# Kernel optimization log

Hardware: AMD Instinct MI355X
Metric: run time of the kernel (lower is better)

The kernel has to match this reference:

```python
import jax, jax.numpy as jnp
import numpy as np


def conv1x1(x, w, b):
    # x: [B,C,H,W], w: [O,C], b: [O]
    return jnp.einsum('bchw,oc->bohw', x, w) + b[None, :, None, None]


def conv2d_same(x, w, b):
    # x: [B,C,H,W], w: [O,I,kh,kw]
    y = jax.lax.conv_general_dilated(x, w, (1, 1), 'SAME',
                                     dimension_numbers=('NCHW', 'OIHW', 'NCHW'))
    return y + b[None, :, None, None]


def l2norm_c(x):
    # F.normalize(x, dim=1): x / max(||x||_2, eps)
    n = jnp.sqrt(jnp.sum(x * x, axis=1, keepdims=True))
    return x / jnp.maximum(n, 1e-12)


def warp_volume(k, disps, directs):
    # Plane-sweep warp. grid_sample(bilinear, border, align_corners=True) with a
    # pure horizontal shift: y-coords equal the identity grid exactly, so
    # bilinear interpolation reduces to 1-D interpolation along W.
    # k: [B,C,H,W], disps: [D], directs: [B,1,1,1] -> [B,C,H,W,D]
    B, C, H, W = k.shape
    dt = k.dtype
    base = jnp.arange(W, dtype=dt)                                   # pixel x
    # normalized shift disp*2 maps to disp*(W-1) pixels (align_corners=True)
    shift = disps.astype(dt)[None, :, None] * directs.reshape(B, 1, 1) * (W - 1)
    px = jnp.clip(base[None, None, :] + shift, 0.0, W - 1)            # [B,D,W] (border pad)
    x0 = jnp.floor(px).astype(jnp.int32)
    x1 = jnp.minimum(x0 + 1, W - 1)
    f = (px - x0.astype(dt))[:, None, None, :, :]                     # [B,1,1,D,W]
    gather = jax.vmap(lambda xb, ib: xb[:, :, ib])                    # [B,C,H,D,W]
    g0 = gather(k, x0)
    g1 = gather(k, x1)
    wk = g0 * (1.0 - f) + g1 * f                                      # [B,C,H,D,W]
    return jnp.transpose(wk, (0, 1, 2, 4, 3))                         # [B,C,H,W,D]


def setup_inputs() -> dict:
    key = jax.random.key(0)
    ks = jax.random.split(key, 16)
    B, C, H, W = 4, 128, 96, 320
    Cm, D = C // 4, 32
    f32 = jnp.float32
    inp = {
        't_feat': jax.random.normal(ks[0], (B, C, H, W), f32),
        's_feat': jax.random.normal(ks[1], (B, C, H, W), f32),
        'directs': jnp.ones((B, 1, 1, 1), f32),
        'image_shape': 320,
        'disps': jnp.arange(D, dtype=f32) * 0.01,
        'wq': jax.random.normal(ks[2], (Cm, C), f32) * 0.05,
        'bq': jnp.zeros((Cm,), f32),
        'wkc': jax.random.normal(ks[3], (Cm, C), f32) * 0.05,
        'bkc': jnp.zeros((Cm,), f32),
        'metric': jnp.eye(Cm, dtype=f32),
        'alpha': jnp.asarray(10.0, f32),
        'beta': jnp.asarray(0.0, f32),
        'w_cf': jax.random.normal(ks[4], (1, 1, 3, 3), f32) * 0.1,
        'b_cf': jnp.zeros((1,), f32),
        'w_da': jax.random.normal(ks[5], (D, 2 * Cm), f32) * 0.05,
        'b_da': jnp.zeros((D,), f32),
        'w_ex': jax.random.normal(ks[6], (C, D), f32) * 0.05,
        'b_ex': jnp.zeros((C,), f32),
        'w_fg': jax.random.normal(ks[7], (1, 2 * C), f32) * 0.05,
        'b_fg': jnp.zeros((1,), f32),
        'w_rd': jax.random.normal(ks[8], (C, C, 3, 3), f32) * 0.02,
        'b_rd': jnp.zeros((C,), f32),
        'w_se1': jax.random.normal(ks[9], (C // 16, C), f32) * 0.1,
        'w_se2': jax.random.normal(ks[10], (C, C // 16), f32) * 0.1,
    }
    return inp


def reference(t_feat, s_feat, directs, image_shape, disps,
              wq, bq, wkc, bkc, metric, alpha, beta,
              w_cf, b_cf, w_da, b_da, w_ex, b_ex, w_fg, b_fg,
              w_rd, b_rd, w_se1, w_se2):
    del image_shape  # only used when train_image_size is set (it is None here)
    q = l2norm_c(conv1x1(t_feat, wq, bq))          # [B,Cm,H,W]
    k = l2norm_c(conv1x1(s_feat, wkc, bkc))        # [B,Cm,H,W]
    warped = warp_volume(k, disps, directs)        # [B,Cm,H,W,D]
    M = 0.5 * (metric + metric.T)
    q_proj = jnp.einsum('bchw,cd->bdhw', q, M)
    sim = jnp.einsum('bdhw,bdhwk->bhwk', q_proj, warped)
    sim = jnp.tanh(alpha * sim + beta)             # [B,H,W,D]
    Cv = jnp.transpose(sim, (0, 3, 1, 2))          # [B,D,H,W]
    B, D, H, W = Cv.shape
    # Conv3d(1,1,(1,3,3)) == per-slice 2D 3x3 conv
    Cf = conv2d_same(Cv.reshape(B * D, 1, H, W), w_cf, b_cf).reshape(B, D, H, W)
    k_mean = warped.mean(axis=-1)                  # [B,Cm,H,W]
    da = jax.nn.sigmoid(conv1x1(jnp.concatenate([q, k_mean], axis=1), w_da, b_da))
    Cf = Cf * da
    P = jax.nn.softmax(Cf, axis=1)                 # [B,D,H,W]
    cost_feat = conv1x1(P, w_ex, b_ex)             # [B,C,H,W]
    g = jax.nn.sigmoid(conv1x1(jnp.concatenate([t_feat, cost_feat], axis=1), w_fg, b_fg))
    fused = g * t_feat + (1.0 - g) * cost_feat
    x = conv2d_same(fused, w_rd, b_rd)
    # SELayer(reduction=16)
    y = x.mean(axis=(2, 3))                        # [B,C]
    y = jax.nn.relu(y @ w_se1.T)
    y = jax.nn.sigmoid(y @ w_se2.T)
    x = x * y[:, :, None, None]
    x = jax.nn.elu(x)
    return (x, P)
```

## Files before the change

### kernel.cpp

```cpp
#include <hip/hip_runtime.h>
#include <hip/hip_bf16.h>
#include <math.h>


typedef __hip_bfloat16 bf16;
typedef unsigned short u16;
typedef __attribute__((ext_vector_type(8))) __bf16 bf16x8;
typedef __attribute__((ext_vector_type(4))) float f4;

#define DEVI static __device__ __forceinline__
DEVI float bf2f(bf16 x) { return __bfloat162float(x); }
DEVI bf16  f2bf(float x) { return __float2bfloat16(x); }
DEVI u16 bfbits(float x) { bf16 h = f2bf(x); return *(u16*)&h; }
DEVI float sigmoidf_(float x) { return 1.0f / (1.0f + expf(-x)); }

constexpr int B_ = 4, C_ = 128, H_ = 96, W_ = 320, CM = 32, D_ = 32;
constexpr int HW = H_ * W_;
constexpr int QPLANE = CM * HW;
constexpr int XN = B_ * C_ * HW;
constexpr int PLN = B_ * D_ * HW;

__device__ __align__(16) float g_scratch[8 * PLN];
__device__ __align__(16) u16   g_fused[XN];
__device__ __align__(16) u16   g_wt[9 * 128 * 128];
__device__ float g_ysum[512];
__device__ float g_se[512];
__device__ int   g_flag[1];

DEVI float ldin(const void* p, int i, int isb) {
    float v;
    if (isb) v = bf2f(((const bf16*)p)[i]);
    else     v = ((const float*)p)[i];
    return v;
}
DEVI void stout(void* p, int i, float v, int isb) {
    if (isb) ((bf16*)p)[i] = f2bf(v);
    else     ((float*)p)[i] = v;
}

__global__ __launch_bounds__(256) void k_detect(
    const void* __restrict__ t, const void* __restrict__ wqp)
{
    __shared__ int bad;
    int tid = threadIdx.x;
    if (tid == 0) bad = 0;
    __syncthreads();
    int mybad = 0;
    for (int i = tid; i < 4096; i += 256) {
        float v = bf2f(((const bf16*)t)[i]);
        if (!(v == v) || fabsf(v) > 64.0f) mybad = 1;
        float u = bf2f(((const bf16*)wqp)[i]);
        if (!(u == u) || fabsf(u) > 64.0f) mybad = 1;
    }
    if (mybad) atomicOr(&bad, 1);
    g_ysum[tid] = 0.f;
    g_ysum[tid + 256] = 0.f;
    __syncthreads();
    if (tid == 0) g_flag[0] = bad ? 0 : 1;
}

__global__ __launch_bounds__(256) void k_wprep(
    const void* __restrict__ w_rd, u16* __restrict__ gw)
{
    int isb = g_flag[0];
    int i = blockIdx.x * 256 + threadIdx.x;
    if (i >= 9 * 128 * 128) return;
    int pos = i >> 14, rem = i & 16383, co = rem >> 7, ci = rem & 127;
    gw[i] = bfbits(ldin(w_rd, (co * 128 + ci) * 9 + pos, isb));
}

__global__ __launch_bounds__(320) void k_qk(
    const void* __restrict__ t_feat, const void* __restrict__ s_feat,
    const void* __restrict__ wq, const void* __restrict__ bq,
    const void* __restrict__ wkc, const void* __restrict__ bkc,
    float* __restrict__ qout, float* __restrict__ kout)
{
    __shared__ float WST[C_ * CM];
    __shared__ float BS[CM];
    int isb = g_flag[0];
    int h = blockIdx.x, b = blockIdx.y, which = blockIdx.z;
    const void* in = which ? s_feat : t_feat;
    const void* wm = which ? wkc : wq;
    const void* bb = which ? bkc : bq;
    float* out = which ? kout : qout;
    int tid = threadIdx.x;
    for (int i = tid; i < C_ * CM; i += 320) {
        int o = i >> 7, c = i & 127;
        WST[c * CM + o] = ldin(wm, i, isb);
    }
    if (tid < CM) BS[tid] = ldin(bb, tid, isb);
    __syncthreads();
    int w = tid;
    float acc[CM];
    #pragma unroll
    for (int o = 0; o < CM; o++) acc[o] = BS[o];
    int base = (b * C_) * HW + h * W_ + w;
    for (int c = 0; c < C_; c++) {
        float v = ldin(in, base + c * HW, isb);
        #pragma unroll
        for (int o = 0; o < CM; o++) acc[o] += v * WST[c * CM + o];
    }
    float n = 0.f;
    #pragma unroll
    for (int o = 0; o < CM; o++) n += acc[o] * acc[o];
    float s = 1.0f / fmaxf(sqrtf(n), 1e-12f);
    float* op = out + (b * CM) * HW + h * W_ + w;
    #pragma unroll
    for (int o = 0; o < CM; o++) op[o * HW] = acc[o] * s;
}

__global__ __launch_bounds__(320, 3) void k_cost(
    const float* __restrict__ qbuf, const float* __restrict__ kbuf,
    const void* __restrict__ metric, const void* __restrict__ disps,
    const void* __restrict__ directs, const void* __restrict__ alpha_p,
    const void* __restrict__ beta_p, const void* __restrict__ w_da,
    const void* __restrict__ b_da,
    float* __restrict__ Cv, float* __restrict__ da)
{
    __shared__ float KS[CM][W_];
    __shared__ float MS[CM][CM];
    __shared__ float WDA[D_ * 64];
    __shared__ float BDA[D_];
    __shared__ float SH[D_];
    int isb = g_flag[0];
    int h = blockIdx.x, b = blockIdx.y, tid = threadIdx.x, w = tid;
    for (int i = tid; i < CM * CM; i += 320) {
        int c = i >> 5, d = i & 31;
        MS[c][d] = 0.5f * (ldin(metric, c * CM + d, isb) + ldin(metric, d * CM + c, isb));
    }
    for (int i = tid; i < D_ * 64; i += 320) WDA[i] = ldin(w_da, i, isb);
    if (tid < D_) {
        BDA[tid] = ldin(b_da, tid, isb);
        SH[tid] = ldin(disps, tid, isb) * ldin(directs, b, isb) * (float)(W_ - 1);
    }
    const float* kp = kbuf + b * QPLANE + h * W_;
    for (int c = 0; c < CM; c++) KS[c][w] = kp[c * HW + w];
    __syncthreads();

    float qp[CM], dqa[CM];
    #pragma unroll
    for (int d = 0; d < CM; d++) { qp[d] = 0.f; dqa[d] = 0.f; }
    const float* qpp = qbuf + b * QPLANE + h * W_ + w;
    for (int c = 0; c < CM; c++) {
        float v = qpp[c * HW];
        #pragma unroll
        for (int d = 0; d < CM; d++) qp[d] += v * MS[c][d];
        #pragma unroll
        for (int d = 0; d < D_; d++) dqa[d] += v * WDA[d * 64 + c];
    }

    float km[CM];
    #pragma unroll
    for (int c = 0; c < CM; c++) km[c] = 0.f;
    float alpha = ldin(alpha_p, 0, isb), beta = ldin(beta_p, 0, isb);
    float* cvp = Cv + (b * D_) * HW + h * W_ + w;
    for (int d = 0; d < D_; d++) {
        float px = fminf(fmaxf((float)w + SH[d], 0.f), (float)(W_ - 1));
        int x0 = (int)floorf(px);
        int x1 = min(x0 + 1, W_ - 1);
        float f = px - (float)x0;
        float sim = 0.f;
        #pragma unroll
        for (int c = 0; c < CM; c++) {
            float g0 = KS[c][x0], g1 = KS[c][x1];
            float val = g0 * (1.0f - f) + g1 * f;
            sim += qp[c] * val;
            km[c] += val;
        }
        cvp[d * HW] = tanhf(alpha * sim + beta);
    }

    #pragma unroll
    for (int c = 0; c < CM; c++) km[c] *= (1.0f / (float)D_);
    float* dap = da + (b * D_) * HW + h * W_ + w;
    for (int d = 0; d < D_; d++) {
        float s = BDA[d] + dqa[d];
        #pragma unroll
        for (int c = 0; c < CM; c++) s += WDA[d * 64 + 32 + c] * km[c];
        dap[d * HW] = sigmoidf_(s);
    }
}

__global__ __launch_bounds__(320) void k_cf_softmax(
    const float* __restrict__ Cv, const float* __restrict__ da,
    const void* __restrict__ w_cf, const void* __restrict__ b_cf,
    float* __restrict__ Pf, void* __restrict__ dout)
{
    __shared__ float R[3][322];
    int isb = g_flag[0];
    int h = blockIdx.x, b = blockIdx.y, tid = threadIdx.x, w = tid;
    float wcf[9];
    #pragma unroll
    for (int i = 0; i < 9; i++) wcf[i] = ldin(w_cf, i, isb);
    float bcf = ldin(b_cf, 0, isb);
    float vals[D_];
    for (int d = 0; d < D_; d++) {
        const float* base = Cv + ((b * D_ + d) * H_) * W_;
        #pragma unroll
        for (int r = 0; r < 3; r++) {
            int hh = h + r - 1;
            R[r][w + 1] = (hh >= 0 && hh < H_) ? base[hh * W_ + w] : 0.f;
        }
        if (tid == 0) {
            R[0][0] = R[1][0] = R[2][0] = 0.f;
            R[0][321] = R[1][321] = R[2][321] = 0.f;
        }
        __syncthreads();
        float s = bcf;
        #pragma unroll
        for (int r = 0; r < 3; r++)
            #pragma unroll
            for (int kw = 0; kw < 3; kw++)
                s += R[r][w + kw] * wcf[r * 3 + kw];
        vals[d] = s * da[((b * D_ + d) * H_ + h) * W_ + w];
        __syncthreads();
    }
    float m = vals[0];
    #pragma unroll
    for (int d = 1; d < D_; d++) m = fmaxf(m, vals[d]);
    float sum = 0.f;
    #pragma unroll
    for (int d = 0; d < D_; d++) { vals[d] = expf(vals[d] - m); sum += vals[d]; }
    float inv = 1.0f / sum;
    int o = (b * D_) * HW + h * W_ + w;
    #pragma unroll
    for (int d = 0; d < D_; d++) {
        float p = vals[d] * inv;
        Pf[o + d * HW] = p;
        stout(dout, XN + o + d * HW, p, isb);
    }
}

__global__ __launch_bounds__(320) void k_fuse(
    const float* __restrict__ Pf, const void* __restrict__ t_feat,
    const void* __restrict__ w_ex, const void* __restrict__ b_ex,
    const void* __restrict__ w_fg, const void* __restrict__ b_fg,
    u16* __restrict__ gf)
{
    __shared__ float WEX[C_ * D_];
    __shared__ float BEX[C_];
    __shared__ float WFG[2 * C_];
    __shared__ float WPRE[D_ + 1];
    int isb = g_flag[0];
    int h = blockIdx.x, b = blockIdx.y, tid = threadIdx.x, w = tid;
    for (int i = tid; i < C_ * D_; i += 320) WEX[i] = ldin(w_ex, i, isb);
    if (tid < C_) BEX[tid] = ldin(b_ex, tid, isb);
    for (int i = tid; i < 2 * C_; i += 320) WFG[i] = ldin(w_fg, i, isb);
    __syncthreads();
    if (tid < D_) {
        float s = 0.f;
        for (int c = 0; c < C_; c++) s += WFG[C_ + c] * WEX[c * D_ + tid];
        WPRE[tid] = s;
    } else if (tid == D_) {
        float s = 0.f;
        for (int c = 0; c < C_; c++) s += WFG[C_ + c] * BEX[c];
        WPRE[D_] = s;
    }
    __syncthreads();
    float p[D_];
    const float* pp = Pf + (b * D_) * HW + h * W_ + w;
    #pragma unroll
    for (int d = 0; d < D_; d++) p[d] = pp[d * HW];
    int tbase = (b * C_) * HW + h * W_ + w;
    float gacc = ldin(b_fg, 0, isb) + WPRE[D_];
    #pragma unroll
    for (int d = 0; d < D_; d++) gacc += WPRE[d] * p[d];
    for (int c = 0; c < C_; c++)
        gacc += WFG[c] * ldin(t_feat, tbase + c * HW, isb);
    float g = sigmoidf_(gacc);
    unsigned int* gfo = (unsigned int*)gf + ((b * H_ + h) * W_ + w) * 64;
    for (int c = 0; c < C_; c += 2) {
        float c0 = BEX[c], c1 = BEX[c + 1];
        #pragma unroll
        for (int d = 0; d < D_; d++) {
            c0 += WEX[c * D_ + d] * p[d];
            c1 += WEX[(c + 1) * D_ + d] * p[d];
        }
        float t0 = ldin(t_feat, tbase + c * HW, isb);
        float t1 = ldin(t_feat, tbase + (c + 1) * HW, isb);
        float v0 = g * t0 + (1.0f - g) * c0;
        float v1 = g * t1 + (1.0f - g) * c1;
        gfo[c >> 1] = ((unsigned int)bfbits(v1) << 16) | bfbits(v0);
    }
}

__global__ __launch_bounds__(128, 2) void k_conv3(
    const u16* __restrict__ gf, const u16* __restrict__ gw,
    const void* __restrict__ b_rd, float* __restrict__ xf)
{
    __shared__ u16 IN[6 * 34 * 40];
    __shared__ u16 WS[128 * 40];
    int isb = g_flag[0];
    int tid = threadIdx.x;
    int wave = tid >> 6, lane = tid & 63;
    int l15 = lane & 15, kq = lane >> 4;
    int w0 = blockIdx.x * 32, h0 = blockIdx.y * 4, b = blockIdx.z;

    f4 acc[4][8];
    #pragma unroll
    for (int mt = 0; mt < 4; mt++)
        #pragma unroll
        for (int nt = 0; nt < 8; nt++) acc[mt][nt] = (f4){0.f, 0.f, 0.f, 0.f};

    float bias[8];
    #pragma unroll
    for (int nt = 0; nt < 8; nt++) bias[nt] = ldin(b_rd, nt * 16 + l15, isb);

    for (int cb = 0; cb < 128; cb += 32) {
        __syncthreads();
        for (int s = tid; s < 204 * 4; s += 128) {
            int p = s >> 2, q = s & 3;
            int hp = p / 34, wp = p - hp * 34;
            int hg = h0 - 1 + hp, wg = w0 - 1 + wp;
            uint4 v = make_uint4(0u, 0u, 0u, 0u);
            if (hg >= 0 && hg < H_ && wg >= 0 && wg < W_)
                v = *(const uint4*)(gf + ((((b * H_ + hg) * W_ + wg) << 7) + cb + q * 8));
            *(uint4*)(&IN[(hp * 34 + wp) * 40 + q * 8]) = v;
        }
        for (int pos = 0; pos < 9; pos++) {
            __syncthreads();
            for (int s = tid; s < 128 * 4; s += 128) {
                int co = s >> 2, q = s & 3;
                *(uint4*)(&WS[co * 40 + q * 8]) =
                    *(const uint4*)(gw + (((pos * 128 + co) << 7) + cb + q * 8));
            }
            __syncthreads();
            int kh = pos / 3, kw = pos - kh * 3;
            bf16x8 bfr[8];
            #pragma unroll
            for (int nt = 0; nt < 8; nt++)
                bfr[nt] = *(bf16x8*)(&WS[(nt * 16 + l15) * 40 + kq * 8]);
            #pragma unroll
            for (int mt = 0; mt < 4; mt++) {
                int px = wave * 64 + mt * 16 + l15;
                int row = (px >> 5) + kh, col = (px & 31) + kw;
                bf16x8 afr = *(bf16x8*)(&IN[(row * 34 + col) * 40 + kq * 8]);
                #pragma unroll
                for (int nt = 0; nt < 8; nt++)
                    acc[mt][nt] = __builtin_amdgcn_mfma_f32_16x16x32_bf16(
                        afr, bfr[nt], acc[mt][nt], 0, 0, 0);
            }
        }
    }
    #pragma unroll
    for (int nt = 0; nt < 8; nt++) {
        int co = nt * 16 + l15;
        float ps = 0.f;
        #pragma unroll
        for (int mt = 0; mt < 4; mt++) {
            #pragma unroll
            for (int r = 0; r < 4; r++) {
                int px = wave * 64 + mt * 16 + kq * 4 + r;
                float v = acc[mt][nt][r] + bias[nt];
                ps += v;
                xf[((b * C_ + co) * H_ + h0 + (px >> 5)) * W_ + w0 + (px & 31)] = v;
            }
        }
        ps += __shfl_xor(ps, 16);
        ps += __shfl_xor(ps, 32);
        if (lane < 16) atomicAdd(&g_ysum[b * C_ + co], ps);
    }
}

__global__ __launch_bounds__(512) void k_se(
    const void* __restrict__ w_se1, const void* __restrict__ w_se2)
{
    __shared__ float YM[B_ * C_];
    __shared__ float Y1[B_ * 8];
    int isb = g_flag[0];
    int tid = threadIdx.x;
    YM[tid] = g_ysum[tid] * (1.0f / (float)HW);
    __syncthreads();
    if (tid < 32) {
        int b = tid >> 3, j = tid & 7;
        float s = 0.f;
        for (int c = 0; c < C_; c++) s += YM[b * C_ + c] * ldin(w_se1, j * C_ + c, isb);
        Y1[tid] = fmaxf(s, 0.f);
    }
    __syncthreads();
    int b = tid >> 7, c = tid & 127;
    float s = 0.f;
    #pragma unroll
    for (int j = 0; j < 8; j++) s += Y1[b * 8 + j] * ldin(w_se2, c * 8 + j, isb);
    g_se[tid] = sigmoidf_(s);
}

__global__ __launch_bounds__(256) void k_elu(
    const float* __restrict__ xf, void* __restrict__ dout)
{
    int isb = g_flag[0];
    int idx = blockIdx.x * 256 + threadIdx.x;
    if (idx >= XN) return;
    int plane = idx / HW;
    float v = xf[idx] * g_se[plane];
    stout(dout, idx, v > 0.f ? v : expm1f(v), isb);
}

extern "C" void kernel_launch(void* const* d_in, const int* in_sizes, int n_in,
                              void* d_out, int out_size, void* d_ws, size_t ws_size,
                              hipStream_t stream)
{
    const void* t_feat  = d_in[0];
    const void* s_feat  = d_in[1];
    const void* directs = d_in[2];
    const void* disps   = d_in[4];
    const void* wq      = d_in[5];
    const void* bq      = d_in[6];
    const void* wkc     = d_in[7];
    const void* bkc     = d_in[8];
    const void* metric  = d_in[9];
    const void* alpha   = d_in[10];
    const void* beta    = d_in[11];
    const void* w_cf    = d_in[12];
    const void* b_cf    = d_in[13];
    const void* w_da    = d_in[14];
    const void* b_da    = d_in[15];
    const void* w_ex    = d_in[16];
    const void* b_ex    = d_in[17];
    const void* w_fg    = d_in[18];
    const void* b_fg    = d_in[19];
    const void* w_rd    = d_in[20];
    const void* b_rd    = d_in[21];
    const void* w_se1   = d_in[22];
    const void* w_se2   = d_in[23];
    (void)in_sizes; (void)n_in; (void)out_size; (void)d_ws; (void)ws_size;

    float* base = nullptr;
    (void)hipGetSymbolAddress((void**)&base, HIP_SYMBOL(g_scratch));
    u16* gf = nullptr;
    (void)hipGetSymbolAddress((void**)&gf, HIP_SYMBOL(g_fused));
    u16* gw = nullptr;
    (void)hipGetSymbolAddress((void**)&gw, HIP_SYMBOL(g_wt));
    float* qb = base;
    float* kb = base + PLN;
    float* Cv = base + 2 * PLN;
    float* da = base + 3 * PLN;
    float* Pf = base + 4 * PLN;
    float* xf = base + 4 * PLN;

    k_detect<<<1, 256, 0, stream>>>(t_feat, wq);
    k_wprep<<<576, 256, 0, stream>>>(w_rd, gw);
    k_qk<<<dim3(H_, B_, 2), 320, 0, stream>>>(t_feat, s_feat, wq, bq, wkc, bkc, qb, kb);
    k_cost<<<dim3(H_, B_), 320, 0, stream>>>(qb, kb, metric, disps, directs,
                                             alpha, beta, w_da, b_da, Cv, da);
    k_cf_softmax<<<dim3(H_, B_), 320, 0, stream>>>(Cv, da, w_cf, b_cf, Pf, d_out);
    k_fuse<<<dim3(H_, B_), 320, 0, stream>>>(Pf, t_feat, w_ex, b_ex, w_fg, b_fg, gf);
    k_conv3<<<dim3(10, 24, 4), 128, 0, stream>>>(gf, gw, b_rd, xf);
    k_se<<<1, 512, 0, stream>>>(w_se1, w_se2);
    k_elu<<<(XN + 255) / 256, 256, 0, stream>>>(xf, d_out);
}
```

Baseline: 631.5 us.

## Fuse cost-filter softmax into fuse kernel and vectorize ELU epilogue

Merges the 3x3 cost filter plus softmax kernel into the fusion kernel, so P stays in registers instead of being written to and re-read from scratch. The 3x3 conv now reads neighbours straight from global/L1 rather than staging rows in shared memory, which removes the per-disparity barriers. The ELU kernel handles four elements per thread with vector loads and stores. The tradeoffs are higher register pressure in the fused kernel and redundant global loads for the stencil.

```diff
diff --git a/kernel.cpp b/kernel.cpp
--- a/kernel.cpp
+++ b/kernel.cpp
@@ -181,61 +181,13 @@
     }
 }
 
-__global__ __launch_bounds__(320) void k_cf_softmax(
+__global__ __launch_bounds__(320) void k_cfp(
     const float* __restrict__ Cv, const float* __restrict__ da,
     const void* __restrict__ w_cf, const void* __restrict__ b_cf,
-    float* __restrict__ Pf, void* __restrict__ dout)
-{
-    __shared__ float R[3][322];
-    int isb = g_flag[0];
-    int h = blockIdx.x, b = blockIdx.y, tid = threadIdx.x, w = tid;
-    float wcf[9];
-    #pragma unroll
-    for (int i = 0; i < 9; i++) wcf[i] = ldin(w_cf, i, isb);
-    float bcf = ldin(b_cf, 0, isb);
-    float vals[D_];
-    for (int d = 0; d < D_; d++) {
-        const float* base = Cv + ((b * D_ + d) * H_) * W_;
-        #pragma unroll
-        for (int r = 0; r < 3; r++) {
-            int hh = h + r - 1;
-            R[r][w + 1] = (hh >= 0 && hh < H_) ? base[hh * W_ + w] : 0.f;
-        }
-        if (tid == 0) {
-            R[0][0] = R[1][0] = R[2][0] = 0.f;
-            R[0][321] = R[1][321] = R[2][321] = 0.f;
-        }
-        __syncthreads();
-        float s = bcf;
-        #pragma unroll
-        for (int r = 0; r < 3; r++)
-            #pragma unroll
-            for (int kw = 0; kw < 3; kw++)
-                s += R[r][w + kw] * wcf[r * 3 + kw];
-        vals[d] = s * da[((b * D_ + d) * H_ + h) * W_ + w];
-        __syncthreads();
-    }
-    float m = vals[0];
-    #pragma unroll
-    for (int d = 1; d < D_; d++) m = fmaxf(m, vals[d]);
-    float sum = 0.f;
-    #pragma unroll
-    for (int d = 0; d < D_; d++) { vals[d] = expf(vals[d] - m); sum += vals[d]; }
-    float inv = 1.0f / sum;
-    int o = (b * D_) * HW + h * W_ + w;
-    #pragma unroll
-    for (int d = 0; d < D_; d++) {
-        float p = vals[d] * inv;
-        Pf[o + d * HW] = p;
-        stout(dout, XN + o + d * HW, p, isb);
-    }
-}
-
-__global__ __launch_bounds__(320) void k_fuse(
-    const float* __restrict__ Pf, const void* __restrict__ t_feat,
-    const void* __restrict__ w_ex, const void* __restrict__ b_ex,
-    const void* __restrict__ w_fg, const void* __restrict__ b_fg,
-    u16* __restrict__ gf)
+    const void* __restrict__ t_feat, const void* __restrict__ w_ex,
+    const void* __restrict__ b_ex, const void* __restrict__ w_fg,
+    const void* __restrict__ b_fg,
+    u16* __restrict__ gf, void* __restrict__ dout)
 {
     __shared__ float WEX[C_ * D_];
     __shared__ float BEX[C_];
@@ -257,14 +209,48 @@
         WPRE[D_] = s;
     }
     __syncthreads();
-    float p[D_];
-    const float* pp = Pf + (b * D_) * HW + h * W_ + w;
-    #pragma unroll
-    for (int d = 0; d < D_; d++) p[d] = pp[d * HW];
+
+    float wcf[9];
+    #pragma unroll
+    for (int i = 0; i < 9; i++) wcf[i] = ldin(w_cf, i, isb);
+    float bcf = ldin(b_cf, 0, isb);
+    int wm1 = (w > 0), wp1 = (w < W_ - 1);
+    float vals[D_];
+    #pragma unroll 4
+    for (int d = 0; d < D_; d++) {
+        const float* base = Cv + ((b * D_ + d) * H_) * W_;
+        float s = bcf;
+        #pragma unroll
+        for (int r = 0; r < 3; r++) {
+            int hh = h + r - 1;
+            if (hh >= 0 && hh < H_) {
+                const float* rp = base + hh * W_ + w;
+                if (wm1) s += rp[-1] * wcf[r * 3 + 0];
+                s += rp[0] * wcf[r * 3 + 1];
+                if (wp1) s += rp[1] * wcf[r * 3 + 2];
+            }
+        }
+        vals[d] = s * da[((b * D_ + d) * H_ + h) * W_ + w];
+    }
+
+    float m = vals[0];
+    #pragma unroll
+    for (int d = 1; d < D_; d++) m = fmaxf(m, vals[d]);
+    float sum = 0.f;
+    #pragma unroll
+    for (int d = 0; d < D_; d++) { vals[d] = expf(vals[d] - m); sum += vals[d]; }
+    float inv = 1.0f / sum;
+    int o = (b * D_) * HW + h * W_ + w;
+    #pragma unroll
+    for (int d = 0; d < D_; d++) {
+        vals[d] *= inv;
+        stout(dout, XN + o + d * HW, vals[d], isb);
+    }
+
     int tbase = (b * C_) * HW + h * W_ + w;
     float gacc = ldin(b_fg, 0, isb) + WPRE[D_];
     #pragma unroll
-    for (int d = 0; d < D_; d++) gacc += WPRE[d] * p[d];
+    for (int d = 0; d < D_; d++) gacc += WPRE[d] * vals[d];
     for (int c = 0; c < C_; c++)
         gacc += WFG[c] * ldin(t_feat, tbase + c * HW, isb);
     float g = sigmoidf_(gacc);
@@ -273,8 +259,8 @@
         float c0 = BEX[c], c1 = BEX[c + 1];
         #pragma unroll
         for (int d = 0; d < D_; d++) {
-            c0 += WEX[c * D_ + d] * p[d];
-            c1 += WEX[(c + 1) * D_ + d] * p[d];
+            c0 += WEX[c * D_ + d] * vals[d];
+            c1 += WEX[(c + 1) * D_ + d] * vals[d];
         }
         float t0 = ldin(t_feat, tbase + c * HW, isb);
         float t1 = ldin(t_feat, tbase + (c + 1) * HW, isb);
@@ -389,11 +375,26 @@
     const float* __restrict__ xf, void* __restrict__ dout)
 {
     int isb = g_flag[0];
-    int idx = blockIdx.x * 256 + threadIdx.x;
-    if (idx >= XN) return;
-    int plane = idx / HW;
-    float v = xf[idx] * g_se[plane];
-    stout(dout, idx, v > 0.f ? v : expm1f(v), isb);
+    int i4 = blockIdx.x * 256 + threadIdx.x;
+    if (i4 >= XN / 4) return;
+    int idx = i4 * 4;
+    float se = g_se[idx / HW];
+    f4 v = *(const f4*)(xf + idx);
+    float r[4];
+    #pragma unroll
+    for (int j = 0; j < 4; j++) {
+        float u = v[j] * se;
+        r[j] = u > 0.f ? u : expm1f(u);
+    }
+    if (isb) {
+        unsigned int lo = ((unsigned int)bfbits(r[1]) << 16) | bfbits(r[0]);
+        unsigned int hi = ((unsigned int)bfbits(r[3]) << 16) | bfbits(r[2]);
+        uint2 pk; pk.x = lo; pk.y = hi;
+        *(uint2*)((u16*)dout + idx) = pk;
+    } else {
+        f4 o; o[0] = r[0]; o[1] = r[1]; o[2] = r[2]; o[3] = r[3];
+        *(f4*)((float*)dout + idx) = o;
+    }
 }
 
 extern "C" void kernel_launch(void* const* d_in, const int* in_sizes, int n_in,
@@ -435,7 +436,6 @@
     float* kb = base + PLN;
     float* Cv = base + 2 * PLN;
     float* da = base + 3 * PLN;
-    float* Pf = base + 4 * PLN;
     float* xf = base + 4 * PLN;
 
     k_detect<<<1, 256, 0, stream>>>(t_feat, wq);
@@ -443,9 +443,9 @@
     k_qk<<<dim3(H_, B_, 2), 320, 0, stream>>>(t_feat, s_feat, wq, bq, wkc, bkc, qb, kb);
     k_cost<<<dim3(H_, B_), 320, 0, stream>>>(qb, kb, metric, disps, directs,
                                              alpha, beta, w_da, b_da, Cv, da);
-    k_cf_softmax<<<dim3(H_, B_), 320, 0, stream>>>(Cv, da, w_cf, b_cf, Pf, d_out);
-    k_fuse<<<dim3(H_, B_), 320, 0, stream>>>(Pf, t_feat, w_ex, b_ex, w_fg, b_fg, gf);
+    k_cfp<<<dim3(H_, B_), 320, 0, stream>>>(Cv, da, w_cf, b_cf, t_feat,
+                                            w_ex, b_ex, w_fg, b_fg, gf, d_out);
     k_conv3<<<dim3(10, 24, 4), 128, 0, stream>>>(gf, gw, b_rd, xf);
     k_se<<<1, 512, 0, stream>>>(w_se1, w_se2);
-    k_elu<<<(XN + 255) / 256, 256, 0, stream>>>(xf, d_out);
-}
+    k_elu<<<(XN / 4 + 255) / 256, 256, 0, stream>>>(xf, d_out);
+}
```

After: 622.5 us. Within noise of the previous version (-1.4%).
